# Kernel optimization log

Measured on AMD Instinct MI355X. Metric: run time of the kernel, lower is better.

Reference implementation:

```python
import jax, jax.numpy as jnp
import numpy as np

B, S, H, E, I, TOPK = 4, 1024, 1024, 8, 2048, 2
SOFT_CAP = 30.0
W_SCALE = 0.02


def setup_inputs() -> dict:
    key = jax.random.key(0)
    k0, k1, k2, k3, k4 = jax.random.split(key, 5)
    return {
        "hidden_states": jax.random.normal(k0, (B, S, H), dtype=jnp.float32),
        "w_gate": jax.random.normal(k1, (E, H), dtype=jnp.float32) * W_SCALE,
        "w1": jax.random.normal(k2, (E, I, H), dtype=jnp.float32) * W_SCALE,
        "w3": jax.random.normal(k3, (E, I, H), dtype=jnp.float32) * W_SCALE,
        "w2": jax.random.normal(k4, (E, H, I), dtype=jnp.float32) * W_SCALE,
        "top_k": TOPK,
    }


def reference(hidden_states, w_gate, w1, w3, w2, top_k):
    orig_shape = hidden_states.shape
    x = hidden_states.reshape(-1, orig_shape[-1])  # [T, H]
    # Router gate + soft cap
    logits = x @ w_gate.T  # [T, E]
    logits = SOFT_CAP * jnp.tanh(logits / SOFT_CAP)
    probs = jax.nn.softmax(logits, axis=-1)
    # top-k routing, renormalize=False -> use softmax probs directly
    top_w, top_i = jax.lax.top_k(probs, top_k)  # [T, k]
    T, nE = probs.shape
    gates = jnp.zeros((T, nE), probs.dtype).at[
        jnp.arange(T)[:, None], top_i
    ].add(top_w)  # [T, E] sparse routing weights
    # Grouped expert GEMMs with gated GELU (GeluAndMul)
    h1 = jnp.einsum('th,eih->tei', x, w1)  # [T, E, I]
    h3 = jnp.einsum('th,eih->tei', x, w3)
    act = jax.nn.gelu(h1, approximate=False) * h3
    y = jnp.einsum('tei,ehi->teh', act, w2)  # [T, E, H]
    out = jnp.einsum('te,teh->th', gates, y)
    return out.reshape(orig_shape)
```

## Files before the change

### kernel.cpp

```cpp
#include <hip/hip_runtime.h>
#include <stdint.h>

#define T_TOK 4096
#define HDIM  1024
#define NEXP  8
#define IDIM  2048
#define BK    64
#define NASSIGN (T_TOK * 2)

typedef short short8 __attribute__((ext_vector_type(8)));
typedef float f32x4 __attribute__((ext_vector_type(4)));

__device__ __forceinline__ unsigned short f32_to_bf16(float f) {
  union { float f; uint32_t u; } v; v.f = f;
  uint32_t r = 0x7FFFu + ((v.u >> 16) & 1u);
  return (unsigned short)((v.u + r) >> 16);
}

__device__ __forceinline__ void gload16(const void* g, void* l) {
  __builtin_amdgcn_global_load_lds(
      (const __attribute__((address_space(1))) uint32_t*)g,
      (__attribute__((address_space(3))) uint32_t*)l, 16, 0, 0);
}

__global__ void cast_w3_kernel(const float* __restrict__ w1,
                               const float* __restrict__ w3,
                               const float* __restrict__ w2,
                               unsigned short* __restrict__ w1b,
                               unsigned short* __restrict__ w3b,
                               unsigned short* __restrict__ w2b, int n8) {
  int i = blockIdx.x * blockDim.x + threadIdx.x;
  if (i >= n8) return;
  const float* src; unsigned short* dst;
  if (blockIdx.y == 0)      { src = w1; dst = w1b; }
  else if (blockIdx.y == 1) { src = w3; dst = w3b; }
  else                      { src = w2; dst = w2b; }
  const float4* s = (const float4*)src + (size_t)i * 2;
  float4 a = s[0], b = s[1];
  short8 o;
  o[0] = f32_to_bf16(a.x); o[1] = f32_to_bf16(a.y);
  o[2] = f32_to_bf16(a.z); o[3] = f32_to_bf16(a.w);
  o[4] = f32_to_bf16(b.x); o[5] = f32_to_bf16(b.y);
  o[6] = f32_to_bf16(b.z); o[7] = f32_to_bf16(b.w);
  ((short8*)dst)[i] = o;
}

__global__ __launch_bounds__(256)
void router_core(const float* __restrict__ x, const float* __restrict__ wg,
                 unsigned short* __restrict__ xb,
                 unsigned char* __restrict__ eids,
                 float* __restrict__ gate_a) {
  __shared__ float wgs[NEXP * HDIM];
  const int tid = threadIdx.x;
#pragma unroll
  for (int i = 0; i < NEXP * HDIM / 4 / 256; ++i)
    ((float4*)wgs)[i * 256 + tid] = ((const float4*)wg)[i * 256 + tid];
  __syncthreads();

  const int wv = tid >> 6, lane = tid & 63;
#pragma unroll
  for (int tt = 0; tt < 2; ++tt) {
    const int t = blockIdx.x * 8 + wv * 2 + tt;
    const float* xr = x + (size_t)t * HDIM;
    float acc0 = 0.f, acc1v = 0.f, acc2 = 0.f, acc3 = 0.f;
    float acc4 = 0.f, acc5 = 0.f, acc6 = 0.f, acc7 = 0.f;
#pragma unroll
    for (int it = 0; it < 4; ++it) {
      const int j = it * 256 + lane * 4;
      const float4 xv = *(const float4*)(xr + j);
      ushort4 u;
      u.x = f32_to_bf16(xv.x); u.y = f32_to_bf16(xv.y);
      u.z = f32_to_bf16(xv.z); u.w = f32_to_bf16(xv.w);
      *(ushort4*)(xb + (size_t)t * HDIM + j) = u;
      const float4 g0 = *(const float4*)(wgs + 0 * HDIM + j);
      const float4 g1 = *(const float4*)(wgs + 1 * HDIM + j);
      const float4 g2 = *(const float4*)(wgs + 2 * HDIM + j);
      const float4 g3 = *(const float4*)(wgs + 3 * HDIM + j);
      const float4 g4 = *(const float4*)(wgs + 4 * HDIM + j);
      const float4 g5 = *(const float4*)(wgs + 5 * HDIM + j);
      const float4 g6 = *(const float4*)(wgs + 6 * HDIM + j);
      const float4 g7 = *(const float4*)(wgs + 7 * HDIM + j);
      acc0 += xv.x * g0.x + xv.y * g0.y + xv.z * g0.z + xv.w * g0.w;
      acc1v += xv.x * g1.x + xv.y * g1.y + xv.z * g1.z + xv.w * g1.w;
      acc2 += xv.x * g2.x + xv.y * g2.y + xv.z * g2.z + xv.w * g2.w;
      acc3 += xv.x * g3.x + xv.y * g3.y + xv.z * g3.z + xv.w * g3.w;
      acc4 += xv.x * g4.x + xv.y * g4.y + xv.z * g4.z + xv.w * g4.w;
      acc5 += xv.x * g5.x + xv.y * g5.y + xv.z * g5.z + xv.w * g5.w;
      acc6 += xv.x * g6.x + xv.y * g6.y + xv.z * g6.z + xv.w * g6.w;
      acc7 += xv.x * g7.x + xv.y * g7.y + xv.z * g7.z + xv.w * g7.w;
    }
    float acc[NEXP] = {acc0, acc1v, acc2, acc3, acc4, acc5, acc6, acc7};
#pragma unroll
    for (int e = 0; e < NEXP; ++e) {
#pragma unroll
      for (int off = 32; off > 0; off >>= 1) acc[e] += __shfl_xor(acc[e], off);
    }
    if (lane == 0) {
      float p[NEXP];
      float mx = -1e30f;
#pragma unroll
      for (int e = 0; e < NEXP; ++e) {
        float l = 30.0f * tanhf(acc[e] * (1.0f / 30.0f));
        p[e] = l;
        mx = fmaxf(mx, l);
      }
      float s = 0.f;
#pragma unroll
      for (int e = 0; e < NEXP; ++e) { p[e] = expf(p[e] - mx); s += p[e]; }
      const float inv = 1.0f / s;
#pragma unroll
      for (int e = 0; e < NEXP; ++e) p[e] *= inv;
      int i0 = 0;
#pragma unroll
      for (int e = 1; e < NEXP; ++e) if (p[e] > p[i0]) i0 = e;
      int i1 = (i0 == 0) ? 1 : 0;
#pragma unroll
      for (int e = 0; e < NEXP; ++e) if (e != i1 && e != i0 && p[e] > p[i1]) i1 = e;
      eids[t * 2]     = (unsigned char)i0;
      gate_a[t * 2]   = p[i0];
      eids[t * 2 + 1] = (unsigned char)i1;
      gate_a[t * 2 + 1] = p[i1];
    }
  }
}

__global__ __launch_bounds__(1024)
void build_lists(const unsigned char* __restrict__ eids,
                 int* __restrict__ counts, int* __restrict__ list) {
  const int e = blockIdx.x;
  const int tid = threadIdx.x;
  const int wid = tid >> 6, lane = tid & 63;
  __shared__ int wave_tot[16];
  __shared__ int running;
  if (tid == 0) running = 0;
  __syncthreads();
#pragma unroll
  for (int c = 0; c < NASSIGN; c += 1024) {
    const int slot = c + tid;
    const bool match = ((int)eids[slot] == e);
    const unsigned long long mask = __ballot(match);
    if (lane == 0) wave_tot[wid] = __popcll(mask);
    __syncthreads();
    int base = running;
    for (int w = 0; w < wid; ++w) base += wave_tot[w];
    if (match) {
      const int pre = __popcll(mask & ((1ull << lane) - 1ull));
      list[e * T_TOK + base + pre] = slot;
    }
    __syncthreads();
    if (tid == 0) {
      int tot = 0;
      for (int w = 0; w < 16; ++w) tot += wave_tot[w];
      running += tot;
    }
    __syncthreads();
  }
  if (tid == 0) counts[e] = running;
}

__global__ __launch_bounds__(256, 2)
void moe_gemm1_fast(const unsigned short* __restrict__ xb,
                    const unsigned short* __restrict__ w1b,
                    const unsigned short* __restrict__ w3b,
                    const int* __restrict__ counts, const int* __restrict__ list,
                    unsigned short* __restrict__ act) {
  const int e = blockIdx.z;
  const int cnt = counts[e];
  const int m0 = blockIdx.y * 128;
  if (m0 >= cnt) return;
  const int n0 = blockIdx.x * 64;

  __shared__ __align__(16) unsigned short As[128 * BK];
  __shared__ __align__(16) unsigned short B1s[64 * BK];
  __shared__ __align__(16) unsigned short B3s[64 * BK];
  __shared__ int entry_l[128];

  const int tid = threadIdx.x;
  if (tid < 128) entry_l[tid] = (m0 + tid < cnt) ? list[e * T_TOK + m0 + tid] : -1;
  __syncthreads();

  const int lane = tid & 63;
  const int l15 = lane & 15;
  const int kg  = lane >> 4;
  const int wv  = tid >> 6;
  const int wvu = __builtin_amdgcn_readfirstlane(wv);
  const int wm = wv >> 1, wn = wv & 1;

  const int srow8  = lane >> 3;
  const int schunk = (lane & 7) ^ srow8;

  const unsigned short* aSrc[4];
#pragma unroll
  for (int r = 0; r < 4; ++r) {
    const int row = r * 32 + wv * 8 + srow8;
    const int en = entry_l[row];
    const int tok = (en >= 0) ? (en >> 1) : 0;
    aSrc[r] = xb + (size_t)tok * HDIM + schunk * 8;
  }
  const unsigned short* b1Src[2];
  const unsigned short* b3Src[2];
#pragma unroll
  for (int r = 0; r < 2; ++r) {
    const int row = r * 32 + wv * 8 + srow8;
    b1Src[r] = w1b + ((size_t)e * IDIM + n0 + row) * HDIM + schunk * 8;
    b3Src[r] = w3b + ((size_t)e * IDIM + n0 + row) * HDIM + schunk * 8;
  }

  int aOff[4][2], bOff[2][2];
#pragma unroll
  for (int mf = 0; mf < 4; ++mf)
#pragma unroll
    for (int ks = 0; ks < 2; ++ks) {
      const int row = wm * 64 + mf * 16 + l15;
      aOff[mf][ks] = row * 128 + (((ks * 4 + kg) ^ (row & 7)) * 16);
    }
#pragma unroll
  for (int nf = 0; nf < 2; ++nf)
#pragma unroll
    for (int ks = 0; ks < 2; ++ks) {
      const int row = wn * 32 + nf * 16 + l15;
      bOff[nf][ks] = row * 128 + (((ks * 4 + kg) ^ (row & 7)) * 16);
    }

  f32x4 acc1[4][2], acc3[4][2];
#pragma unroll
  for (int mf = 0; mf < 4; ++mf)
#pragma unroll
    for (int nf = 0; nf < 2; ++nf) {
      acc1[mf][nf] = (f32x4){0.f, 0.f, 0.f, 0.f};
      acc3[mf][nf] = (f32x4){0.f, 0.f, 0.f, 0.f};
    }

  const char* AsB = (const char*)As;
  const char* B1B = (const char*)B1s;
  const char* B3B = (const char*)B3s;

  for (int k0 = 0; k0 < HDIM; k0 += BK) {
#pragma unroll
    for (int r = 0; r < 4; ++r) gload16(aSrc[r], As + r * 2048 + wvu * 512);
#pragma unroll
    for (int r = 0; r < 2; ++r) {
      gload16(b1Src[r], B1s + r * 2048 + wvu * 512);
      gload16(b3Src[r], B3s + r * 2048 + wvu * 512);
    }
#pragma unroll
    for (int r = 0; r < 4; ++r) aSrc[r] += BK;
#pragma unroll
    for (int r = 0; r < 2; ++r) { b1Src[r] += BK; b3Src[r] += BK; }
    __syncthreads();

    short8 af[4][2], b1f[2][2], b3f[2][2];
#pragma unroll
    for (int mf = 0; mf < 4; ++mf)
#pragma unroll
      for (int ks = 0; ks < 2; ++ks)
        af[mf][ks] = *(const short8*)(AsB + aOff[mf][ks]);
#pragma unroll
    for (int nf = 0; nf < 2; ++nf)
#pragma unroll
      for (int ks = 0; ks < 2; ++ks) {
        b1f[nf][ks] = *(const short8*)(B1B + bOff[nf][ks]);
        b3f[nf][ks] = *(const short8*)(B3B + bOff[nf][ks]);
      }
#pragma unroll
    for (int mf = 0; mf < 4; ++mf)
#pragma unroll
      for (int nf = 0; nf < 2; ++nf)
#pragma unroll
        for (int ks = 0; ks < 2; ++ks) {
          acc1[mf][nf] = __builtin_amdgcn_mfma_f32_16x16x32_bf16(af[mf][ks], b1f[nf][ks], acc1[mf][nf], 0, 0, 0);
          acc3[mf][nf] = __builtin_amdgcn_mfma_f32_16x16x32_bf16(af[mf][ks], b3f[nf][ks], acc3[mf][nf], 0, 0, 0);
        }
    __syncthreads();
  }

#pragma unroll
  for (int mf = 0; mf < 4; ++mf) {
#pragma unroll
    for (int i = 0; i < 4; ++i) {
      const int r = wm * 64 + mf * 16 + kg * 4 + i;
      const int en = entry_l[r];
      if (en < 0) continue;
      unsigned short* arow = act + (size_t)en * IDIM + n0 + wn * 32;
#pragma unroll
      for (int nf = 0; nf < 2; ++nf) {
        const float h1 = acc1[mf][nf][i];
        const float h3 = acc3[mf][nf][i];
        const float g = 0.5f * h1 * (1.0f + erff(h1 * 0.70710678118f));
        arow[nf * 16 + l15] = f32_to_bf16(g * h3);
      }
    }
  }
}

__global__ __launch_bounds__(256, 2)
void moe_gemm2_fast(const unsigned short* __restrict__ act,
                    const unsigned short* __restrict__ w2b,
                    const int* __restrict__ counts, const int* __restrict__ list,
                    const float* __restrict__ gate_a,
                    float* __restrict__ out) {
  const int e = blockIdx.z;
  const int cnt = counts[e];
  const int m0 = blockIdx.y * 128;
  if (m0 >= cnt) return;
  const int n0 = blockIdx.x * 128;

  __shared__ __align__(16) unsigned short As[128 * BK];
  __shared__ __align__(16) unsigned short Bs[128 * BK];
  __shared__ int entry_l[128];

  const int tid = threadIdx.x;
  if (tid < 128) entry_l[tid] = (m0 + tid < cnt) ? list[e * T_TOK + m0 + tid] : -1;
  __syncthreads();

  const int lane = tid & 63;
  const int l15 = lane & 15;
  const int kg  = lane >> 4;
  const int wv  = tid >> 6;
  const int wvu = __builtin_amdgcn_readfirstlane(wv);
  const int wm = wv >> 1, wn = wv & 1;

  const int srow8  = lane >> 3;
  const int schunk = (lane & 7) ^ srow8;

  const unsigned short* aSrc[4];
  const unsigned short* bSrc[4];
#pragma unroll
  for (int r = 0; r < 4; ++r) {
    const int row = r * 32 + wv * 8 + srow8;
    const int en = entry_l[row];
    const int arow = (en >= 0) ? en : 0;
    aSrc[r] = act + (size_t)arow * IDIM + schunk * 8;
    bSrc[r] = w2b + ((size_t)e * HDIM + n0 + row) * IDIM + schunk * 8;
  }

  int aOff[4][2], bOff[4][2];
#pragma unroll
  for (int mf = 0; mf < 4; ++mf)
#pragma unroll
    for (int ks = 0; ks < 2; ++ks) {
      const int row = wm * 64 + mf * 16 + l15;
      aOff[mf][ks] = row * 128 + (((ks * 4 + kg) ^ (row & 7)) * 16);
    }
#pragma unroll
  for (int nf = 0; nf < 4; ++nf)
#pragma unroll
    for (int ks = 0; ks < 2; ++ks) {
      const int row = wn * 64 + nf * 16 + l15;
      bOff[nf][ks] = row * 128 + (((ks * 4 + kg) ^ (row & 7)) * 16);
    }

  f32x4 acc[4][4];
#pragma unroll
  for (int mf = 0; mf < 4; ++mf)
#pragma unroll
    for (int nf = 0; nf < 4; ++nf) acc[mf][nf] = (f32x4){0.f, 0.f, 0.f, 0.f};

  const char* AsB = (const char*)As;
  const char* BsB = (const char*)Bs;

  for (int k0 = 0; k0 < IDIM; k0 += BK) {
#pragma unroll
    for (int r = 0; r < 4; ++r) {
      gload16(aSrc[r], As + r * 2048 + wvu * 512);
      gload16(bSrc[r], Bs + r * 2048 + wvu * 512);
    }
#pragma unroll
    for (int r = 0; r < 4; ++r) { aSrc[r] += BK; bSrc[r] += BK; }
    __syncthreads();

    short8 af[4][2], bf[4][2];
#pragma unroll
    for (int mf = 0; mf < 4; ++mf)
#pragma unroll
      for (int ks = 0; ks < 2; ++ks)
        af[mf][ks] = *(const short8*)(AsB + aOff[mf][ks]);
#pragma unroll
    for (int nf = 0; nf < 4; ++nf)
#pragma unroll
      for (int ks = 0; ks < 2; ++ks)
        bf[nf][ks] = *(const short8*)(BsB + bOff[nf][ks]);
#pragma unroll
    for (int mf = 0; mf < 4; ++mf)
#pragma unroll
      for (int nf = 0; nf < 4; ++nf)
#pragma unroll
        for (int ks = 0; ks < 2; ++ks)
          acc[mf][nf] = __builtin_amdgcn_mfma_f32_16x16x32_bf16(af[mf][ks], bf[nf][ks], acc[mf][nf], 0, 0, 0);
    __syncthreads();
  }

#pragma unroll
  for (int mf = 0; mf < 4; ++mf) {
#pragma unroll
    for (int i = 0; i < 4; ++i) {
      const int r = wm * 64 + mf * 16 + kg * 4 + i;
      const int en = entry_l[r];
      if (en < 0) continue;
      const float gate = gate_a[en];
      float* orow = out + (size_t)(en >> 1) * HDIM + n0 + wn * 64;
#pragma unroll
      for (int nf = 0; nf < 4; ++nf)
        atomicAdd(&orow[nf * 16 + l15], acc[mf][nf][i] * gate);
    }
  }
}

#define LSTRIDE 40

__global__ __launch_bounds__(256, 2)
void moe_gemm1_fb(const unsigned short* __restrict__ xb,
                  const float* __restrict__ w1, const float* __restrict__ w3,
                  const int* __restrict__ counts, const int* __restrict__ list,
                  unsigned short* __restrict__ act) {
  const int e = blockIdx.z;
  const int cnt = counts[e];
  const int m0 = blockIdx.y * 128;
  if (m0 >= cnt) return;
  const int n0 = blockIdx.x * 64;

  __shared__ short As[128 * LSTRIDE];
  __shared__ short B1s[64 * LSTRIDE];
  __shared__ short B3s[64 * LSTRIDE];
  __shared__ int entry_l[128];

  const int tid = threadIdx.x;
  if (tid < 128) entry_l[tid] = (m0 + tid < cnt) ? list[e * T_TOK + m0 + tid] : -1;
  __syncthreads();

  const int lane = tid & 63;
  const int l15 = lane & 15;
  const int kg = lane >> 4;
  const int wv = tid >> 6;
  const int wm = wv >> 1, wn = wv & 1;

  f32x4 acc1[4][2], acc3[4][2];
#pragma unroll
  for (int mf = 0; mf < 4; ++mf)
#pragma unroll
    for (int nf = 0; nf < 2; ++nf) {
      acc1[mf][nf] = (f32x4){0.f, 0.f, 0.f, 0.f};
      acc3[mf][nf] = (f32x4){0.f, 0.f, 0.f, 0.f};
    }

  const int srow = tid >> 2;
  const int scol = (tid & 3) << 3;

  const float* w1base = w1 + ((size_t)e * IDIM + n0) * HDIM;
  const float* w3base = w3 + ((size_t)e * IDIM + n0) * HDIM;

  for (int k0 = 0; k0 < HDIM; k0 += 32) {
#pragma unroll
    for (int it = 0; it < 2; ++it) {
      const int r = srow + it * 64;
      const int en = entry_l[r];
      uint4 v = {0u, 0u, 0u, 0u};
      if (en >= 0)
        v = *(const uint4*)(xb + ((size_t)(en >> 1) * HDIM + k0 + scol));
      *(uint4*)(&As[r * LSTRIDE + scol]) = v;
    }
    {
      const float* p1 = w1base + (size_t)srow * HDIM + k0 + scol;
      float4 a0 = *(const float4*)(p1);
      float4 a1 = *(const float4*)(p1 + 4);
      short8 sb;
      sb[0] = f32_to_bf16(a0.x); sb[1] = f32_to_bf16(a0.y);
      sb[2] = f32_to_bf16(a0.z); sb[3] = f32_to_bf16(a0.w);
      sb[4] = f32_to_bf16(a1.x); sb[5] = f32_to_bf16(a1.y);
      sb[6] = f32_to_bf16(a1.z); sb[7] = f32_to_bf16(a1.w);
      *(short8*)(&B1s[srow * LSTRIDE + scol]) = sb;
      const float* p3 = w3base + (size_t)srow * HDIM + k0 + scol;
      float4 c0 = *(const float4*)(p3);
      float4 c1 = *(const float4*)(p3 + 4);
      sb[0] = f32_to_bf16(c0.x); sb[1] = f32_to_bf16(c0.y);
      sb[2] = f32_to_bf16(c0.z); sb[3] = f32_to_bf16(c0.w);
      sb[4] = f32_to_bf16(c1.x); sb[5] = f32_to_bf16(c1.y);
      sb[6] = f32_to_bf16(c1.z); sb[7] = f32_to_bf16(c1.w);
      *(short8*)(&B3s[srow * LSTRIDE + scol]) = sb;
    }
    __syncthreads();
    short8 af[4], b1f[2], b3f[2];
#pragma unroll
    for (int mf = 0; mf < 4; ++mf)
      af[mf] = *(const short8*)(&As[(wm * 64 + mf * 16 + l15) * LSTRIDE + kg * 8]);
#pragma unroll
    for (int nf = 0; nf < 2; ++nf) {
      b1f[nf] = *(const short8*)(&B1s[(wn * 32 + nf * 16 + l15) * LSTRIDE + kg * 8]);
      b3f[nf] = *(const short8*)(&B3s[(wn * 32 + nf * 16 + l15) * LSTRIDE + kg * 8]);
    }
#pragma unroll
    for (int mf = 0; mf < 4; ++mf)
#pragma unroll
      for (int nf = 0; nf < 2; ++nf) {
        acc1[mf][nf] = __builtin_amdgcn_mfma_f32_16x16x32_bf16(af[mf], b1f[nf], acc1[mf][nf], 0, 0, 0);
        acc3[mf][nf] = __builtin_amdgcn_mfma_f32_16x16x32_bf16(af[mf], b3f[nf], acc3[mf][nf], 0, 0, 0);
      }
    __syncthreads();
  }

#pragma unroll
  for (int mf = 0; mf < 4; ++mf) {
#pragma unroll
    for (int i = 0; i < 4; ++i) {
      const int r = wm * 64 + mf * 16 + kg * 4 + i;
      const int en = entry_l[r];
      if (en < 0) continue;
      unsigned short* arow = act + (size_t)en * IDIM + n0 + wn * 32;
#pragma unroll
      for (int nf = 0; nf < 2; ++nf) {
        const float h1 = acc1[mf][nf][i];
        const float h3 = acc3[mf][nf][i];
        const float g = 0.5f * h1 * (1.0f + erff(h1 * 0.70710678118f));
        arow[nf * 16 + l15] = f32_to_bf16(g * h3);
      }
    }
  }
}

__global__ __launch_bounds__(256, 2)
void moe_gemm2_fb(const unsigned short* __restrict__ act,
                  const float* __restrict__ w2,
                  const int* __restrict__ counts, const int* __restrict__ list,
                  const float* __restrict__ gate_a,
                  float* __restrict__ out) {
  const int e = blockIdx.z;
  const int cnt = counts[e];
  const int m0 = blockIdx.y * 128;
  if (m0 >= cnt) return;
  const int n0 = blockIdx.x * 64;

  __shared__ short As[128 * LSTRIDE];
  __shared__ short Bs[64 * LSTRIDE];
  __shared__ int entry_l[128];

  const int tid = threadIdx.x;
  if (tid < 128) entry_l[tid] = (m0 + tid < cnt) ? list[e * T_TOK + m0 + tid] : -1;
  __syncthreads();

  const int lane = tid & 63;
  const int l15 = lane & 15;
  const int kg = lane >> 4;
  const int wv = tid >> 6;
  const int wm = wv >> 1, wn = wv & 1;

  f32x4 acc[4][2];
#pragma unroll
  for (int mf = 0; mf < 4; ++mf)
#pragma unroll
    for (int nf = 0; nf < 2; ++nf) acc[mf][nf] = (f32x4){0.f, 0.f, 0.f, 0.f};

  const int srow = tid >> 2;
  const int scol = (tid & 3) << 3;

  const float* w2base = w2 + ((size_t)e * IDIM + n0) * IDIM;

  const float* w2b2 = w2 + ((size_t)e * HDIM + n0) * IDIM;

  for (int k0 = 0; k0 < IDIM; k0 += 32) {
#pragma unroll
    for (int it = 0; it < 2; ++it) {
      const int r = srow + it * 64;
      const int en = entry_l[r];
      uint4 v = {0u, 0u, 0u, 0u};
      if (en >= 0)
        v = *(const uint4*)(act + ((size_t)en * IDIM + k0 + scol));
      *(uint4*)(&As[r * LSTRIDE + scol]) = v;
    }
    {
      const float* p2 = w2b2 + (size_t)srow * IDIM + k0 + scol;
      float4 a0 = *(const float4*)(p2);
      float4 a1 = *(const float4*)(p2 + 4);
      short8 sb;
      sb[0] = f32_to_bf16(a0.x); sb[1] = f32_to_bf16(a0.y);
      sb[2] = f32_to_bf16(a0.z); sb[3] = f32_to_bf16(a0.w);
      sb[4] = f32_to_bf16(a1.x); sb[5] = f32_to_bf16(a1.y);
      sb[6] = f32_to_bf16(a1.z); sb[7] = f32_to_bf16(a1.w);
      *(short8*)(&Bs[srow * LSTRIDE + scol]) = sb;
    }
    __syncthreads();
    short8 af[4], bf[2];
#pragma unroll
    for (int mf = 0; mf < 4; ++mf)
      af[mf] = *(const short8*)(&As[(wm * 64 + mf * 16 + l15) * LSTRIDE + kg * 8]);
#pragma unroll
    for (int nf = 0; nf < 2; ++nf)
      bf[nf] = *(const short8*)(&Bs[(wn * 32 + nf * 16 + l15) * LSTRIDE + kg * 8]);
#pragma unroll
    for (int mf = 0; mf < 4; ++mf)
#pragma unroll
      for (int nf = 0; nf < 2; ++nf)
        acc[mf][nf] = __builtin_amdgcn_mfma_f32_16x16x32_bf16(af[mf], bf[nf], acc[mf][nf], 0, 0, 0);
    __syncthreads();
  }

#pragma unroll
  for (int mf = 0; mf < 4; ++mf) {
#pragma unroll
    for (int i = 0; i < 4; ++i) {
      const int r = wm * 64 + mf * 16 + kg * 4 + i;
      const int en = entry_l[r];
      if (en < 0) continue;
      const float gate = gate_a[en];
      float* orow = out + (size_t)(en >> 1) * HDIM + n0 + wn * 32;
#pragma unroll
      for (int nf = 0; nf < 2; ++nf)
        atomicAdd(&orow[nf * 16 + l15], acc[mf][nf][i] * gate);
    }
  }
}

extern "C" void kernel_launch(void* const* d_in, const int* in_sizes, int n_in,
                              void* d_out, int out_size, void* d_ws, size_t ws_size,
                              hipStream_t stream) {
  const float* x  = (const float*)d_in[0];
  const float* wg = (const float*)d_in[1];
  const float* w1 = (const float*)d_in[2];
  const float* w3 = (const float*)d_in[3];
  const float* w2 = (const float*)d_in[4];
  float* out = (float*)d_out;

  char* ws = (char*)d_ws;
  int*            counts = (int*)ws;
  int*            list   = (int*)(ws + 1024);
  float*          gate_a = (float*)(ws + 132096);
  unsigned char*  eids   = (unsigned char*)(ws + 165888);
  unsigned short* xb     = (unsigned short*)(ws + 262144);
  const size_t OFF_ACT = 262144 + (size_t)T_TOK * HDIM * 2;
  unsigned short* act    = (unsigned short*)(ws + OFF_ACT);
  const size_t WELEMS = (size_t)NEXP * IDIM * HDIM;
  const size_t OFF_W1B = OFF_ACT + (size_t)2 * T_TOK * IDIM * 2;
  const size_t OFF_W3B = OFF_W1B + WELEMS * 2;
  const size_t OFF_W2B = OFF_W3B + WELEMS * 2;
  const size_t WS_NEED = OFF_W2B + WELEMS * 2;

  hipMemsetAsync(d_out, 0, (size_t)out_size * sizeof(float), stream);

  router_core<<<T_TOK / 8, 256, 0, stream>>>(x, wg, xb, eids, gate_a);
  build_lists<<<NEXP, 1024, 0, stream>>>(eids, counts, list);

  if (ws_size >= WS_NEED) {
    unsigned short* w1b = (unsigned short*)(ws + OFF_W1B);
    unsigned short* w3b = (unsigned short*)(ws + OFF_W3B);
    unsigned short* w2b = (unsigned short*)(ws + OFF_W2B);
    const int n8 = (int)(WELEMS / 8);
    cast_w3_kernel<<<dim3((n8 + 255) / 256, 3), 256, 0, stream>>>(w1, w3, w2, w1b, w3b, w2b, n8);
    moe_gemm1_fast<<<dim3(IDIM / 64, T_TOK / 128, NEXP), 256, 0, stream>>>(xb, w1b, w3b, counts, list, act);
    moe_gemm2_fast<<<dim3(HDIM / 128, T_TOK / 128, NEXP), 256, 0, stream>>>(act, w2b, counts, list, gate_a, out);
  } else {
    moe_gemm1_fb<<<dim3(IDIM / 64, T_TOK / 128, NEXP), 256, 0, stream>>>(xb, w1, w3, counts, list, act);
    moe_gemm2_fb<<<dim3(HDIM / 64, T_TOK / 128, NEXP), 256, 0, stream>>>(act, w2, counts, list, gate_a, out);
  }
}
```

Before: 243.8 us.

## Double GEMM M-tile to 256 rows and replace atomic scatter with combine pass

Both expert GEMMs now use 512-thread blocks covering 256 routed rows. Each block reuses every loaded weight tile across twice as many tokens, which halves weight traffic from global memory per token. The second GEMM now writes gated per-assignment outputs to a scratch buffer (reusing the w1 bf16 region) instead of doing float atomicAdd into the output. A new combine kernel then sums the two assignments per token, which also removes the output memset. The trade-offs are an extra 32 MB write plus a read pass, and more wasted work in partially filled 256-row tiles.

```diff
diff --git a/kernel.cpp b/kernel.cpp
--- a/kernel.cpp
+++ b/kernel.cpp
@@ -158,7 +158,7 @@
   if (tid == 0) counts[e] = running;
 }
 
-__global__ __launch_bounds__(256, 2)
+__global__ __launch_bounds__(512, 2)
 void moe_gemm1_fast(const unsigned short* __restrict__ xb,
                     const unsigned short* __restrict__ w1b,
                     const unsigned short* __restrict__ w3b,
@@ -166,25 +166,25 @@
                     unsigned short* __restrict__ act) {
   const int e = blockIdx.z;
   const int cnt = counts[e];
-  const int m0 = blockIdx.y * 128;
+  const int m0 = blockIdx.y * 256;
   if (m0 >= cnt) return;
   const int n0 = blockIdx.x * 64;
 
-  __shared__ __align__(16) unsigned short As[128 * BK];
+  __shared__ __align__(16) unsigned short As[256 * BK];
   __shared__ __align__(16) unsigned short B1s[64 * BK];
   __shared__ __align__(16) unsigned short B3s[64 * BK];
-  __shared__ int entry_l[128];
+  __shared__ int entry_l[256];
 
   const int tid = threadIdx.x;
-  if (tid < 128) entry_l[tid] = (m0 + tid < cnt) ? list[e * T_TOK + m0 + tid] : -1;
+  if (tid < 256) entry_l[tid] = (m0 + tid < cnt) ? list[e * T_TOK + m0 + tid] : -1;
   __syncthreads();
 
   const int lane = tid & 63;
   const int l15 = lane & 15;
   const int kg  = lane >> 4;
-  const int wv  = tid >> 6;
-  const int wvu = __builtin_amdgcn_readfirstlane(wv);
-  const int wm = wv >> 1, wn = wv & 1;
+  const int wid = tid >> 6;
+  const int wvu = __builtin_amdgcn_readfirstlane(wid);
+  const int wm = wid >> 1, wn = wid & 1;
 
   const int srow8  = lane >> 3;
   const int schunk = (lane & 7) ^ srow8;
@@ -192,19 +192,13 @@
   const unsigned short* aSrc[4];
 #pragma unroll
   for (int r = 0; r < 4; ++r) {
-    const int row = r * 32 + wv * 8 + srow8;
+    const int row = r * 64 + wid * 8 + srow8;
     const int en = entry_l[row];
     const int tok = (en >= 0) ? (en >> 1) : 0;
     aSrc[r] = xb + (size_t)tok * HDIM + schunk * 8;
   }
-  const unsigned short* b1Src[2];
-  const unsigned short* b3Src[2];
-#pragma unroll
-  for (int r = 0; r < 2; ++r) {
-    const int row = r * 32 + wv * 8 + srow8;
-    b1Src[r] = w1b + ((size_t)e * IDIM + n0 + row) * HDIM + schunk * 8;
-    b3Src[r] = w3b + ((size_t)e * IDIM + n0 + row) * HDIM + schunk * 8;
-  }
+  const unsigned short* b1Src = w1b + ((size_t)e * IDIM + n0 + wid * 8 + srow8) * HDIM + schunk * 8;
+  const unsigned short* b3Src = w3b + ((size_t)e * IDIM + n0 + wid * 8 + srow8) * HDIM + schunk * 8;
 
   int aOff[4][2], bOff[2][2];
 #pragma unroll
@@ -237,16 +231,12 @@
 
   for (int k0 = 0; k0 < HDIM; k0 += BK) {
 #pragma unroll
-    for (int r = 0; r < 4; ++r) gload16(aSrc[r], As + r * 2048 + wvu * 512);
-#pragma unroll
-    for (int r = 0; r < 2; ++r) {
-      gload16(b1Src[r], B1s + r * 2048 + wvu * 512);
-      gload16(b3Src[r], B3s + r * 2048 + wvu * 512);
-    }
+    for (int r = 0; r < 4; ++r) gload16(aSrc[r], As + r * 4096 + wvu * 512);
+    gload16(b1Src, B1s + wvu * 512);
+    gload16(b3Src, B3s + wvu * 512);
 #pragma unroll
     for (int r = 0; r < 4; ++r) aSrc[r] += BK;
-#pragma unroll
-    for (int r = 0; r < 2; ++r) { b1Src[r] += BK; b3Src[r] += BK; }
+    b1Src += BK; b3Src += BK;
     __syncthreads();
 
     short8 af[4][2], b1f[2][2], b3f[2][2];
@@ -293,44 +283,48 @@
   }
 }
 
-__global__ __launch_bounds__(256, 2)
+__global__ __launch_bounds__(512, 2)
 void moe_gemm2_fast(const unsigned short* __restrict__ act,
                     const unsigned short* __restrict__ w2b,
                     const int* __restrict__ counts, const int* __restrict__ list,
                     const float* __restrict__ gate_a,
-                    float* __restrict__ out) {
+                    float* __restrict__ ybuf) {
   const int e = blockIdx.z;
   const int cnt = counts[e];
-  const int m0 = blockIdx.y * 128;
+  const int m0 = blockIdx.y * 256;
   if (m0 >= cnt) return;
   const int n0 = blockIdx.x * 128;
 
-  __shared__ __align__(16) unsigned short As[128 * BK];
+  __shared__ __align__(16) unsigned short As[256 * BK];
   __shared__ __align__(16) unsigned short Bs[128 * BK];
-  __shared__ int entry_l[128];
+  __shared__ int entry_l[256];
 
   const int tid = threadIdx.x;
-  if (tid < 128) entry_l[tid] = (m0 + tid < cnt) ? list[e * T_TOK + m0 + tid] : -1;
+  if (tid < 256) entry_l[tid] = (m0 + tid < cnt) ? list[e * T_TOK + m0 + tid] : -1;
   __syncthreads();
 
   const int lane = tid & 63;
   const int l15 = lane & 15;
   const int kg  = lane >> 4;
-  const int wv  = tid >> 6;
-  const int wvu = __builtin_amdgcn_readfirstlane(wv);
-  const int wm = wv >> 1, wn = wv & 1;
+  const int wid = tid >> 6;
+  const int wvu = __builtin_amdgcn_readfirstlane(wid);
+  const int wm = wid >> 1, wn = wid & 1;
 
   const int srow8  = lane >> 3;
   const int schunk = (lane & 7) ^ srow8;
 
   const unsigned short* aSrc[4];
-  const unsigned short* bSrc[4];
 #pragma unroll
   for (int r = 0; r < 4; ++r) {
-    const int row = r * 32 + wv * 8 + srow8;
+    const int row = r * 64 + wid * 8 + srow8;
     const int en = entry_l[row];
     const int arow = (en >= 0) ? en : 0;
     aSrc[r] = act + (size_t)arow * IDIM + schunk * 8;
+  }
+  const unsigned short* bSrc[2];
+#pragma unroll
+  for (int r = 0; r < 2; ++r) {
+    const int row = r * 64 + wid * 8 + srow8;
     bSrc[r] = w2b + ((size_t)e * HDIM + n0 + row) * IDIM + schunk * 8;
   }
 
@@ -361,12 +355,13 @@
 
   for (int k0 = 0; k0 < IDIM; k0 += BK) {
 #pragma unroll
-    for (int r = 0; r < 4; ++r) {
-      gload16(aSrc[r], As + r * 2048 + wvu * 512);
-      gload16(bSrc[r], Bs + r * 2048 + wvu * 512);
-    }
-#pragma unroll
-    for (int r = 0; r < 4; ++r) { aSrc[r] += BK; bSrc[r] += BK; }
+    for (int r = 0; r < 4; ++r) gload16(aSrc[r], As + r * 4096 + wvu * 512);
+#pragma unroll
+    for (int r = 0; r < 2; ++r) gload16(bSrc[r], Bs + r * 4096 + wvu * 512);
+#pragma unroll
+    for (int r = 0; r < 4; ++r) aSrc[r] += BK;
+#pragma unroll
+    for (int r = 0; r < 2; ++r) bSrc[r] += BK;
     __syncthreads();
 
     short8 af[4][2], bf[4][2];
@@ -398,12 +393,24 @@
       const int en = entry_l[r];
       if (en < 0) continue;
       const float gate = gate_a[en];
-      float* orow = out + (size_t)(en >> 1) * HDIM + n0 + wn * 64;
+      float* yrow = ybuf + (size_t)en * HDIM + n0 + wn * 64;
 #pragma unroll
       for (int nf = 0; nf < 4; ++nf)
-        atomicAdd(&orow[nf * 16 + l15], acc[mf][nf][i] * gate);
-    }
-  }
+        yrow[nf * 16 + l15] = acc[mf][nf][i] * gate;
+    }
+  }
+}
+
+__global__ __launch_bounds__(256)
+void combine_kernel(const float* __restrict__ ybuf, float* __restrict__ out) {
+  const int i = blockIdx.x * 256 + threadIdx.x;
+  const int t  = i >> 8;
+  const int j4 = i & 255;
+  const float4 a = ((const float4*)(ybuf + (size_t)(2 * t) * HDIM))[j4];
+  const float4 b = ((const float4*)(ybuf + (size_t)(2 * t + 1) * HDIM))[j4];
+  float4 o;
+  o.x = a.x + b.x; o.y = a.y + b.y; o.z = a.z + b.z; o.w = a.w + b.w;
+  ((float4*)out)[i] = o;
 }
 
 #define LSTRIDE 40
@@ -552,8 +559,6 @@
   const int srow = tid >> 2;
   const int scol = (tid & 3) << 3;
 
-  const float* w2base = w2 + ((size_t)e * IDIM + n0) * IDIM;
-
   const float* w2b2 = w2 + ((size_t)e * HDIM + n0) * IDIM;
 
   for (int k0 = 0; k0 < IDIM; k0 += 32) {
@@ -633,8 +638,6 @@
   const size_t OFF_W2B = OFF_W3B + WELEMS * 2;
   const size_t WS_NEED = OFF_W2B + WELEMS * 2;
 
-  hipMemsetAsync(d_out, 0, (size_t)out_size * sizeof(float), stream);
-
   router_core<<<T_TOK / 8, 256, 0, stream>>>(x, wg, xb, eids, gate_a);
   build_lists<<<NEXP, 1024, 0, stream>>>(eids, counts, list);
 
@@ -642,11 +645,14 @@
     unsigned short* w1b = (unsigned short*)(ws + OFF_W1B);
     unsigned short* w3b = (unsigned short*)(ws + OFF_W3B);
     unsigned short* w2b = (unsigned short*)(ws + OFF_W2B);
+    float* ybuf = (float*)(ws + OFF_W1B);
     const int n8 = (int)(WELEMS / 8);
     cast_w3_kernel<<<dim3((n8 + 255) / 256, 3), 256, 0, stream>>>(w1, w3, w2, w1b, w3b, w2b, n8);
-    moe_gemm1_fast<<<dim3(IDIM / 64, T_TOK / 128, NEXP), 256, 0, stream>>>(xb, w1b, w3b, counts, list, act);
-    moe_gemm2_fast<<<dim3(HDIM / 128, T_TOK / 128, NEXP), 256, 0, stream>>>(act, w2b, counts, list, gate_a, out);
+    moe_gemm1_fast<<<dim3(IDIM / 64, T_TOK / 256, NEXP), 512, 0, stream>>>(xb, w1b, w3b, counts, list, act);
+    moe_gemm2_fast<<<dim3(HDIM / 128, T_TOK / 256, NEXP), 512, 0, stream>>>(act, w2b, counts, list, gate_a, ybuf);
+    combine_kernel<<<T_TOK * HDIM / 4 / 256, 256, 0, stream>>>(ybuf, out);
   } else {
+    hipMemsetAsync(d_out, 0, (size_t)out_size * sizeof(float), stream);
     moe_gemm1_fb<<<dim3(IDIM / 64, T_TOK / 128, NEXP), 256, 0, stream>>>(xb, w1, w3, counts, list, act);
     moe_gemm2_fb<<<dim3(HDIM / 64, T_TOK / 128, NEXP), 256, 0, stream>>>(act, w2, counts, list, gate_a, out);
   }
```

After: 231.2 us. -5.1%, faster.
